# Optimization experiments

Hardware: AMD Instinct MI355X
Metric: run time of the kernel (lower is better)

The kernel has to match this reference:

```python
import jax, jax.numpy as jnp
import numpy as np

N_NODES = 10000
N_EDGES = 100000
C = 64          # in_channels == out_channels (required by x_i + x_m)
D_EDGE = 16     # edge_attr feature dim


def setup_inputs() -> dict:
    key = jax.random.key(0)
    k_x, k_ei, k_ea, k_w, k_b, k_r, k_bias = jax.random.split(key, 7)
    x = jax.random.normal(k_x, (N_NODES, C), dtype=jnp.float32)
    edge_index = jax.random.randint(k_ei, (2, N_EDGES), 0, N_NODES, dtype=jnp.int32)
    edge_attr = jax.random.normal(k_ea, (N_EDGES, D_EDGE), dtype=jnp.float32)
    # nn = Linear(D_EDGE -> C*C), producing per-edge [C, C] weight matrices
    W_nn = jax.random.normal(k_w, (D_EDGE, C * C), dtype=jnp.float32) * (1.0 / np.sqrt(D_EDGE))
    b_nn = jax.random.normal(k_b, (C * C,), dtype=jnp.float32) * 0.01
    root = jax.random.normal(k_r, (C, C), dtype=jnp.float32) * (1.0 / np.sqrt(C))
    bias = jax.random.normal(k_bias, (C,), dtype=jnp.float32) * 0.01
    return {"x": x, "edge_index": edge_index, "edge_attr": edge_attr,
            "W_nn": W_nn, "b_nn": b_nn, "root": root, "bias": bias}


def reference(x, edge_index, edge_attr, W_nn, b_nn, root, bias):
    N, Cc = x.shape
    row, col = edge_index[0], edge_index[1]
    # per-edge weight matrices from nn(edge_attr): [E, C, C]
    e = (edge_attr @ W_nn + b_nn).reshape(-1, Cc, Cc)
    # gather source features and apply edge-conditioned matmul: [E, C]
    m = jnp.einsum('ec,eco->eo', x[row], e)
    # Faithful to torch loop: x_m[i] = m[col == i].mean() -> SCALAR mean over
    # all elements of incoming messages, broadcast across the feature row.
    seg_sum = jax.ops.segment_sum(m.sum(axis=1), col, num_segments=N)       # [N]
    cnt = jax.ops.segment_sum(jnp.ones_like(col, dtype=x.dtype), col,
                              num_segments=N) * Cc                            # [N]
    mean = jnp.where(cnt > 0, seg_sum / jnp.maximum(cnt, 1.0), 0.0)          # [N]
    x_m = jnp.broadcast_to(mean[:, None], (N, Cc))                            # [N, C]
    # root transform + bias
    out = x @ root + bias + x_m
    return out
```

## Files before the change

kernel.cpp:

```cpp
#include <hip/hip_runtime.h>
#include <hip/hip_bf16.h>


#define CC 64
#define DE 16
#define PAD 65

__global__ __launch_bounds__(256) void k_edge_direct(const float* __restrict__ W,
                                                     const float* __restrict__ b,
                                                     const float* __restrict__ x,
                                                     const int* __restrict__ ei,
                                                     const float* __restrict__ ea,
                                                     float* __restrict__ seg,
                                                     float* __restrict__ cnt,
                                                     int E) {
    __shared__ float ws[1024 + CC];
    const int tid = threadIdx.x;

    for (int p = tid; p < 1024 + CC; p += 256) {
        const float4* src = (p < 1024) ? (const float4*)(W + (size_t)p * CC)
                                       : (const float4*)(b + (size_t)(p - 1024) * CC);
        float s = 0.f;
#pragma unroll
        for (int i = 0; i < 16; ++i) { float4 v = src[i]; s += v.x + v.y + v.z + v.w; }
        ws[p] = s;
    }
    __syncthreads();

    int e = blockIdx.x * 256 + tid;
    if (e >= E) return;

    const int r  = ei[e];
    const int cn = ei[E + e];

    const float4* a4 = (const float4*)(ea + (size_t)e * DE);
    float4 av[4];
#pragma unroll
    for (int i = 0; i < 4; ++i) av[i] = a4[i];
    float eas[DE] = { av[0].x, av[0].y, av[0].z, av[0].w,
                      av[1].x, av[1].y, av[1].z, av[1].w,
                      av[2].x, av[2].y, av[2].z, av[2].w,
                      av[3].x, av[3].y, av[3].z, av[3].w };

    const float4* ws4 = (const float4*)ws;
    const float4* bs4 = (const float4*)(ws + 1024);
    float4 u[16];
#pragma unroll
    for (int c4 = 0; c4 < 16; ++c4) u[c4] = bs4[c4];
#pragma unroll
    for (int d = 0; d < DE; ++d) {
        float ed = eas[d];
#pragma unroll
        for (int c4 = 0; c4 < 16; ++c4) {
            float4 w = ws4[d * 16 + c4];
            u[c4].x += ed * w.x; u[c4].y += ed * w.y;
            u[c4].z += ed * w.z; u[c4].w += ed * w.w;
        }
    }

    const float4* x4 = (const float4*)(x + (size_t)r * CC);
    float s = 0.f;
#pragma unroll
    for (int c4 = 0; c4 < 16; ++c4) {
        float4 xv = x4[c4];
        s += u[c4].x * xv.x + u[c4].y * xv.y + u[c4].z * xv.z + u[c4].w * xv.w;
    }

    atomicAdd(seg + cn, s);
    atomicAdd(cnt + cn, 1.0f);
}

__global__ __launch_bounds__(256) void k_final(const float* __restrict__ x,
                                               const float* __restrict__ root,
                                               const float* __restrict__ bias,
                                               const float* __restrict__ seg,
                                               const float* __restrict__ cnt,
                                               float* __restrict__ out,
                                               int N) {
    __shared__ float rt[CC * CC];
    __shared__ float xs[16 * PAD];
    __shared__ float bi[CC];
    __shared__ float mn[16];
    int tid = threadIdx.x;
    int n0 = blockIdx.x * 16;

#pragma unroll
    for (int i = 0; i < 16; ++i) rt[tid + i * 256] = root[tid + i * 256];
#pragma unroll
    for (int it = 0; it < 4; ++it) {
        int i = it * 256 + tid;
        if ((size_t)n0 * CC + i < (size_t)N * CC)
            xs[(i >> 6) * PAD + (i & 63)] = x[(size_t)n0 * CC + i];
    }
    if (tid < CC) bi[tid] = bias[tid];
    if (tid < 16 && n0 + tid < N) {
        float c = cnt[n0 + tid];
        mn[tid] = c > 0.f ? seg[n0 + tid] / (c * (float)CC) : 0.f;
    }
    __syncthreads();

    int nl = tid >> 4, ci = tid & 15;
    int n = n0 + nl;
    if (n >= N) return;

    const float4* rt4 = (const float4*)rt;
    const float4* bi4 = (const float4*)bi;
    float m = mn[nl];
    float4 bv = bi4[ci];
    float4 acc = make_float4(bv.x + m, bv.y + m, bv.z + m, bv.w + m);
#pragma unroll
    for (int k = 0; k < CC; ++k) {
        float a  = xs[nl * PAD + k];
        float4 w = rt4[k * 16 + ci];
        acc.x += a * w.x; acc.y += a * w.y; acc.z += a * w.z; acc.w += a * w.w;
    }
    *(float4*)(out + (size_t)n * CC + ci * 4) = acc;
}

extern "C" void kernel_launch(void* const* d_in, const int* in_sizes, int n_in,
                              void* d_out, int out_size, void* d_ws, size_t ws_size,
                              hipStream_t stream) {
    const float* x    = (const float*)d_in[0];
    const int*   ei   = (const int*)  d_in[1];
    const float* ea   = (const float*)d_in[2];
    const float* W    = (const float*)d_in[3];
    const float* b    = (const float*)d_in[4];
    const float* root = (const float*)d_in[5];
    const float* bias = (const float*)d_in[6];
    float* out = (float*)d_out;
    float* ws  = (float*)d_ws;

    const int N = in_sizes[0] / CC;
    const int E = in_sizes[1] / 2;

    float* seg = ws;
    float* cnt = ws + N;

    int eBlocks = (E + 255) / 256;
    int fBlocks = (N + 15) / 16;

    k_edge_direct<<<eBlocks, 256, 0, stream>>>(W, b, x, ei, ea, seg, cnt, E);
    k_final      <<<fBlocks, 256, 0, stream>>>(x, root, bias, seg, cnt, out, N);
}
```

Before: 105.3 us.

## Precompute per-node projections so edge kernel does a 16-wide dot product

Reorders the per-edge contraction so that each source node's features are first projected through the row-summed edge weights, giving a 16-value vector plus a bias scalar per node. The edge kernel then only gathers that small vector, dots it with the edge attributes and performs the atomics. Per-edge arithmetic drops from about a thousand multiply-adds to sixteen, and the per-edge gather shrinks from 64 floats to 17. The cost is an extra kernel launch and an extra intermediate buffer in workspace.

```diff
diff --git a/kernel.cpp b/kernel.cpp
--- a/kernel.cpp
+++ b/kernel.cpp
@@ -6,64 +6,83 @@
 #define DE 16
 #define PAD 65
 
-__global__ __launch_bounds__(256) void k_edge_direct(const float* __restrict__ W,
-                                                     const float* __restrict__ b,
-                                                     const float* __restrict__ x,
-                                                     const int* __restrict__ ei,
-                                                     const float* __restrict__ ea,
-                                                     float* __restrict__ seg,
-                                                     float* __restrict__ cnt,
-                                                     int E) {
+__global__ __launch_bounds__(128) void k_node_v(const float* __restrict__ W,
+                                                const float* __restrict__ b,
+                                                const float* __restrict__ x,
+                                                float* __restrict__ v,
+                                                float* __restrict__ bx,
+                                                int N) {
     __shared__ float ws[1024 + CC];
     const int tid = threadIdx.x;
 
-    for (int p = tid; p < 1024 + CC; p += 256) {
+    for (int p = tid; p < 1024 + CC; p += 128) {
         const float4* src = (p < 1024) ? (const float4*)(W + (size_t)p * CC)
                                        : (const float4*)(b + (size_t)(p - 1024) * CC);
         float s = 0.f;
 #pragma unroll
-        for (int i = 0; i < 16; ++i) { float4 v = src[i]; s += v.x + v.y + v.z + v.w; }
+        for (int i = 0; i < 16; ++i) { float4 t = src[i]; s += t.x + t.y + t.z + t.w; }
         ws[p] = s;
     }
     __syncthreads();
 
-    int e = blockIdx.x * 256 + tid;
+    int n = blockIdx.x * 128 + tid;
+    if (n >= N) return;
+
+    const float4* x4 = (const float4*)(x + (size_t)n * CC);
+    float4 xv[16];
+#pragma unroll
+    for (int i = 0; i < 16; ++i) xv[i] = x4[i];
+
+    const float4* ws4 = (const float4*)ws;
+    const float4* bs4 = (const float4*)(ws + 1024);
+
+    float bs = 0.f;
+#pragma unroll
+    for (int c4 = 0; c4 < 16; ++c4) {
+        float4 w = bs4[c4];
+        bs += w.x * xv[c4].x + w.y * xv[c4].y + w.z * xv[c4].z + w.w * xv[c4].w;
+    }
+    bx[n] = bs;
+
+    float vd[DE];
+#pragma unroll
+    for (int d = 0; d < DE; ++d) {
+        float s = 0.f;
+#pragma unroll
+        for (int c4 = 0; c4 < 16; ++c4) {
+            float4 w = ws4[d * 16 + c4];
+            s += w.x * xv[c4].x + w.y * xv[c4].y + w.z * xv[c4].z + w.w * xv[c4].w;
+        }
+        vd[d] = s;
+    }
+    float4* vo = (float4*)(v + (size_t)n * DE);
+#pragma unroll
+    for (int i = 0; i < 4; ++i)
+        vo[i] = make_float4(vd[4 * i], vd[4 * i + 1], vd[4 * i + 2], vd[4 * i + 3]);
+}
+
+__global__ __launch_bounds__(256) void k_edge(const int* __restrict__ ei,
+                                              const float* __restrict__ ea,
+                                              const float* __restrict__ v,
+                                              const float* __restrict__ bx,
+                                              float* __restrict__ seg,
+                                              float* __restrict__ cnt,
+                                              int E) {
+    int e = blockIdx.x * 256 + threadIdx.x;
     if (e >= E) return;
 
     const int r  = ei[e];
     const int cn = ei[E + e];
 
     const float4* a4 = (const float4*)(ea + (size_t)e * DE);
-    float4 av[4];
+    const float4* v4 = (const float4*)(v + (size_t)r * DE);
+
+    float s = bx[r];
 #pragma unroll
-    for (int i = 0; i < 4; ++i) av[i] = a4[i];
-    float eas[DE] = { av[0].x, av[0].y, av[0].z, av[0].w,
-                      av[1].x, av[1].y, av[1].z, av[1].w,
-                      av[2].x, av[2].y, av[2].z, av[2].w,
-                      av[3].x, av[3].y, av[3].z, av[3].w };
-
-    const float4* ws4 = (const float4*)ws;
-    const float4* bs4 = (const float4*)(ws + 1024);
-    float4 u[16];
-#pragma unroll
-    for (int c4 = 0; c4 < 16; ++c4) u[c4] = bs4[c4];
-#pragma unroll
-    for (int d = 0; d < DE; ++d) {
-        float ed = eas[d];
-#pragma unroll
-        for (int c4 = 0; c4 < 16; ++c4) {
-            float4 w = ws4[d * 16 + c4];
-            u[c4].x += ed * w.x; u[c4].y += ed * w.y;
-            u[c4].z += ed * w.z; u[c4].w += ed * w.w;
-        }
-    }
-
-    const float4* x4 = (const float4*)(x + (size_t)r * CC);
-    float s = 0.f;
-#pragma unroll
-    for (int c4 = 0; c4 < 16; ++c4) {
-        float4 xv = x4[c4];
-        s += u[c4].x * xv.x + u[c4].y * xv.y + u[c4].z * xv.z + u[c4].w * xv.w;
+    for (int i = 0; i < 4; ++i) {
+        float4 a = a4[i];
+        float4 w = v4[i];
+        s += a.x * w.x + a.y * w.y + a.z * w.z + a.w * w.w;
     }
 
     atomicAdd(seg + cn, s);
@@ -135,10 +154,14 @@
 
     float* seg = ws;
     float* cnt = ws + N;
+    float* v   = ws + 2 * N;
+    float* bx  = ws + 2 * N + (size_t)N * DE;
 
+    int vBlocks = (N + 127) / 128;
     int eBlocks = (E + 255) / 256;
     int fBlocks = (N + 15) / 16;
 
-    k_edge_direct<<<eBlocks, 256, 0, stream>>>(W, b, x, ei, ea, seg, cnt, E);
-    k_final      <<<fBlocks, 256, 0, stream>>>(x, root, bias, seg, cnt, out, N);
+    k_node_v<<<vBlocks, 128, 0, stream>>>(W, b, x, v, bx, N);
+    k_edge  <<<eBlocks, 256, 0, stream>>>(ei, ea, v, bx, seg, cnt, E);
+    k_final <<<fBlocks, 256, 0, stream>>>(x, root, bias, seg, cnt, out, N);
 }
```

Result: no change. 106.7 us (+1.3%).
